# Optimization experiments

Hardware: AMD Instinct MI355X
Metric: run time of the kernel (lower is better)

Reference implementation:

```python
import jax
import jax.numpy as jnp
import numpy as np
from jax import lax

KSIZE = 3
C = 32


def _conv3x3(x, w):
    # NCHW input, OIHW weight, stride 1, padding 1 (matches nn.Conv2d(padding=1))
    return lax.conv_general_dilated(
        x, w, window_strides=(1, 1), padding=((1, 1), (1, 1)),
        dimension_numbers=("NCHW", "OIHW", "NCHW"))


def setup_inputs() -> dict:
    key = jax.random.key(0)
    k1, k2, k3 = jax.random.split(key, 3)
    N, H, W = 2, 64, 64
    x = jax.random.normal(k1, (N, C, H, W), dtype=jnp.float32)
    # conv1: C -> C, 3x3; PyTorch default init scale ~ 1/sqrt(fan_in)
    conv1_w = jax.random.normal(k2, (C, C, 3, 3), dtype=jnp.float32) * (1.0 / np.sqrt(C * 9))
    # conv2: C -> C*C*9, 3x3
    conv2_w = jax.random.normal(k3, (C * C * KSIZE * KSIZE, C, 3, 3), dtype=jnp.float32) * (1.0 / np.sqrt(C * 9))
    return {"x": x, "conv1_w": conv1_w, "conv2_w": conv2_w}


def reference(x, conv1_w, conv2_w):
    N, _, H, W = x.shape
    # kernel-generation branch: conv -> relu -> conv -> tanh
    h = jax.nn.relu(_conv3x3(x, conv1_w))
    rst = _conv3x3(h, conv2_w)  # [N, C*C*9, H, W]
    weight = jnp.tanh(rst.reshape(N, C, C, H, W, KSIZE, KSIZE))
    # non-uniform conv apply: per-pixel CxC 3x3 kernel, pad=1
    xp = jnp.pad(x, ((0, 0), (0, 0), (1, 1), (1, 1)))
    # patches[n, ci, h, w, kh, kw] = xp[n, ci, h+kh, w+kw]
    patches = jnp.stack(
        [xp[:, :, kh:kh + H, kw:kw + W] for kh in range(KSIZE) for kw in range(KSIZE)],
        axis=-1).reshape(N, C, H, W, KSIZE, KSIZE)
    out = jnp.einsum("noihwkl,nihwkl->nohw", weight, patches)
    return out
```

## Files before the change

kernel.cpp:

```cpp
#include <hip/hip_runtime.h>

typedef unsigned int uint;
typedef unsigned short ushort_t;

#define CN 32
#define HW 4096
#define KDIM 288
#define PDIM 8192
#define NB 2

typedef __attribute__((ext_vector_type(8))) short bf16x8;
typedef __attribute__((ext_vector_type(4))) float f32x4;

static __device__ __forceinline__ ushort_t f2bf(float f) {
    uint u = __float_as_uint(f);
    uint r = (u + 0x7fffu + ((u >> 16) & 1u)) >> 16;
    return (ushort_t)r;
}

static __device__ __forceinline__ void gl_lds16(const void* g, void* l) {
    __builtin_amdgcn_global_load_lds(
        (const __attribute__((address_space(1))) unsigned int*)g,
        (__attribute__((address_space(3))) unsigned int*)l, 16, 0, 0);
}

static __device__ __forceinline__ float fast_tanh(float v) {
    float e = __expf(2.0f * v);
    return 1.0f - 2.0f * __builtin_amdgcn_rcpf(e + 1.0f);
}


__global__ __launch_bounds__(256) void prep_kernel(
    const float* __restrict__ x, const float* __restrict__ w1,
    const float* __restrict__ w2, float* __restrict__ hout,
    ushort_t* __restrict__ A_bf, float4* __restrict__ out_zero)
{
    __shared__ float w1s[KDIM];
    int bb = blockIdx.x;
    if (bb < 256) {
        int c = (bb >> 2) & 31;
        int n = bb >> 7;
        for (int j = threadIdx.x; j < KDIM; j += 256) w1s[j] = w1[c * KDIM + j];
        __syncthreads();

        int idx = bb * 256 + threadIdx.x;
        int ws0 = (idx & 15) * 4;
        int hh  = (idx >> 4) & 63;

        float acc0 = 0.f, acc1 = 0.f, acc2 = 0.f, acc3 = 0.f;
        for (int ci = 0; ci < CN; ci++) {
            const float* xp = x + (((size_t)(n * CN + ci)) << 12);
            #pragma unroll
            for (int kh = 0; kh < 3; kh++) {
                int y = hh + kh - 1;
                if ((unsigned)y >= 64u) continue;
                const float* row = xp + (y << 6);
                float4 v = *(const float4*)(row + ws0);
                float left  = (ws0 > 0)  ? row[ws0 - 1] : 0.f;
                float right = (ws0 < 60) ? row[ws0 + 4] : 0.f;
                float rb[6] = {left, v.x, v.y, v.z, v.w, right};
                const float* wp = &w1s[ci * 9 + kh * 3];
                #pragma unroll
                for (int kw = 0; kw < 3; kw++) {
                    float wgt = wp[kw];
                    acc0 = fmaf(wgt, rb[0 + kw], acc0);
                    acc1 = fmaf(wgt, rb[1 + kw], acc1);
                    acc2 = fmaf(wgt, rb[2 + kw], acc2);
                    acc3 = fmaf(wgt, rb[3 + kw], acc3);
                }
            }
        }
        float4 o = make_float4(fmaxf(acc0, 0.f), fmaxf(acc1, 0.f),
                               fmaxf(acc2, 0.f), fmaxf(acc3, 0.f));
        *(float4*)(hout + (((size_t)(n * CN + c)) << 12) + (hh << 6) + ws0) = o;
    } else {
        int idx = (bb - 256) * 256 + threadIdx.x;
        if (idx < 65536)
            out_zero[idx] = make_float4(0.f, 0.f, 0.f, 0.f);
        int row = idx / 36;
        int cw  = idx - row * 36;
        int g = cw >> 2, s = cw & 3;
        const float* base = w2 + (size_t)row * KDIM + g * 32;
        float4 lo = *(const float4*)(base + s * 4);
        float4 hi = *(const float4*)(base + 16 + s * 4);
        alignas(16) ushort_t o[8] = {f2bf(lo.x), f2bf(lo.y), f2bf(lo.z), f2bf(lo.w),
                                     f2bf(hi.x), f2bf(hi.y), f2bf(hi.z), f2bf(hi.w)};
        *(uint4*)(A_bf + (size_t)idx * 8) = *(const uint4*)o;
    }
}

__global__ __launch_bounds__(256) void im2col_bf16_perm(
    const float* __restrict__ h, ushort_t* __restrict__ Bm)
{
    int idx = blockIdx.x * 256 + threadIdx.x;
    int p  = idx / 36;
    int cw = idx - p * 36;
    int g = cw >> 2, s = cw & 3;
    int n  = p >> 12;
    int sp = p & 4095;
    int hh = sp >> 6;
    int w  = sp & 63;
    const float* hn = h + (((size_t)n * CN) << 12);
    alignas(16) ushort_t o[8];
    #pragma unroll
    for (int j = 0; j < 8; j++) {
        int ko = (j < 4) ? (s * 4 + j) : (12 + s * 4 + j);
        int k  = g * 32 + ko;
        int ci = (k * 57) >> 9;
        int kk = k - ci * 9;
        int kh = (kk * 11) >> 5;
        int kw = kk - kh * 3;
        int y  = hh + kh - 1;
        int xw = w + kw - 1;
        float v = 0.f;
        if ((unsigned)y < 64u && (unsigned)xw < 64u)
            v = hn[((size_t)ci << 12) + (y << 6) + xw];
        o[j] = f2bf(v);
    }
    *(uint4*)(Bm + (size_t)idx * 8) = *(const uint4*)o;
}

__global__ __launch_bounds__(512, 4) void fused_gemm_apply(
    const ushort_t* __restrict__ A, const ushort_t* __restrict__ B,
    const float* __restrict__ x, float* __restrict__ out)
{
    __shared__ ushort_t AL[2][128 * 32];
    __shared__ ushort_t BL[2][256 * 32];
    __shared__ float vred[4][256];

    int tid = threadIdx.x;
    int bid = blockIdx.x;
    int sb  = (bid & 7) * 288 + (bid >> 3);
    int tw  = sb % 144;
    int cg  = (sb / 144) & 7;
    int n   = sb / 1152;

    int lane = tid & 63, wv = tid >> 6;
    int wm = wv >> 2, wt = wv & 3;
    int i16 = lane & 15, kg = lane >> 4;

    int T0 = tw * 256;
    int c8 = T0 >> 12;
    int q0 = T0 & 4095;

    int cA = tid;
    int rA = cA >> 2;
    int k8A = (((cA & 3) ^ ((cA >> 3) & 3)) << 3);
    const ushort_t* srcA = A +
        (size_t)((cg * 4 + (rA >> 5)) * KDIM + (rA & 31) * 9 + c8) * KDIM + k8A;
    int cB0 = tid, cB1 = 512 + tid;
    int rB0 = cB0 >> 2, rB1 = cB1 >> 2;
    int k8B0 = (((cB0 & 3) ^ ((cB0 >> 3) & 3)) << 3);
    int k8B1 = (((cB1 & 3) ^ ((cB1 >> 3) & 3)) << 3);
    const ushort_t* srcB0 = B + (size_t)((n << 12) + q0 + rB0) * KDIM + k8B0;
    const ushort_t* srcB1 = B + (size_t)((n << 12) + q0 + rB1) * KDIM + k8B1;
    int dstA = wv * 512;
    int dstB0 = wv * 512, dstB1 = 4096 + wv * 512;

    f32x4 acc[4][4] = {};

    gl_lds16(srcA,  &AL[0][dstA]);
    gl_lds16(srcB0, &BL[0][dstB0]);
    gl_lds16(srcB1, &BL[0][dstB1]);

    #pragma unroll
    for (int ks = 0; ks < 9; ks++) {
        int cur = ks & 1;
        if (ks < 8) {
            int k0 = (ks + 1) * 32;
            gl_lds16(srcA + k0,  &AL[cur ^ 1][dstA]);
            gl_lds16(srcB0 + k0, &BL[cur ^ 1][dstB0]);
            gl_lds16(srcB1 + k0, &BL[cur ^ 1][dstB1]);
            __builtin_amdgcn_sched_barrier(0);
            asm volatile("s_waitcnt vmcnt(3)" ::: "memory");
        } else {
            __builtin_amdgcn_sched_barrier(0);
            asm volatile("s_waitcnt vmcnt(0)" ::: "memory");
        }
        __builtin_amdgcn_sched_barrier(0);
        __builtin_amdgcn_s_barrier();
        __builtin_amdgcn_sched_barrier(0);

        bf16x8 af[4], bfr[4];
        #pragma unroll
        for (int mf = 0; mf < 4; mf++) {
            int row = wm * 64 + mf * 16 + i16;
            af[mf] = *(const bf16x8*)
                &AL[cur][row * 32 + ((kg ^ ((row >> 1) & 3)) << 3)];
        }
        #pragma unroll
        for (int nf = 0; nf < 4; nf++) {
            int row = wt * 64 + nf * 16 + i16;
            bfr[nf] = *(const bf16x8*)
                &BL[cur][row * 32 + ((kg ^ ((row >> 1) & 3)) << 3)];
        }
        #pragma unroll
        for (int mf = 0; mf < 4; mf++)
            #pragma unroll
            for (int nf = 0; nf < 4; nf++)
                acc[mf][nf] = __builtin_amdgcn_mfma_f32_16x16x32_bf16(
                    af[mf], bfr[nf], acc[mf][nf], 0, 0, 0);

        __builtin_amdgcn_sched_barrier(0);
        asm volatile("s_waitcnt lgkmcnt(0)" ::: "memory");
        __builtin_amdgcn_sched_barrier(0);
        __builtin_amdgcn_s_barrier();
        __builtin_amdgcn_sched_barrier(0);
    }

    const float* xn = x + (((size_t)n * CN) << 12);
    #pragma unroll
    for (int nf = 0; nf < 4; nf++) {
        int t  = T0 + wt * 64 + nf * 16 + i16;
        uint sp = ((uint)t * 58255u) >> 19;
        int kk = t - (int)sp * 9;
        int kh = (kk * 11) >> 5;
        int kw = kk - kh * 3;
        int y  = (int)(sp >> 6) + kh - 1;
        int xw = (int)(sp & 63) + kw - 1;
        bool ok = ((unsigned)y < 64u) && ((unsigned)xw < 64u);
        int poff = (y << 6) + xw;
        float xa[4], xb[4];
        #pragma unroll
        for (int r = 0; r < 4; r++) {
            int cia = kg * 4 + r;
            xa[r] = ok ? xn[((size_t)cia << 12) + poff] : 0.f;
            xb[r] = ok ? xn[((size_t)(cia + 16) << 12) + poff] : 0.f;
        }
        float s0 = 0.f, s1 = 0.f;
        #pragma unroll
        for (int r = 0; r < 4; r++) {
            s0 = fmaf(fast_tanh(acc[0][nf][r]), xa[r], s0);
            s0 = fmaf(fast_tanh(acc[1][nf][r]), xb[r], s0);
            s1 = fmaf(fast_tanh(acc[2][nf][r]), xa[r], s1);
            s1 = fmaf(fast_tanh(acc[3][nf][r]), xb[r], s1);
        }
        s0 += __shfl_xor(s0, 16); s0 += __shfl_xor(s0, 32);
        s1 += __shfl_xor(s1, 16); s1 += __shfl_xor(s1, 32);
        if (kg == 0) {
            vred[2 * wm + 0][wt * 64 + nf * 16 + i16] = s0;
            vred[2 * wm + 1][wt * 64 + nf * 16 + i16] = s1;
        }
    }
    __syncthreads();

    if (tid < 128) {
        int g  = tid >> 5, bi = tid & 31;
        uint spA = ((uint)T0 * 58255u) >> 19;
        int sp = (int)spA + bi;
        int lo = sp * 9;     if (lo < T0) lo = T0;
        int hi = sp * 9 + 9; if (hi > T0 + 256) hi = T0 + 256;
        if (lo < hi) {
            float s = 0.f;
            for (int t = lo; t < hi; t++) s += vred[g][t - T0];
            atomicAdd(&out[(((size_t)n * CN + cg * 4 + g) << 12) + sp], s);
        }
    }
}

extern "C" void kernel_launch(void* const* d_in, const int* in_sizes, int n_in,
                              void* d_out, int out_size, void* d_ws, size_t ws_size,
                              hipStream_t stream) {
    const float* x  = (const float*)d_in[0];
    const float* w1 = (const float*)d_in[1];
    const float* w2 = (const float*)d_in[2];
    float* out = (float*)d_out;
    char* ws = (char*)d_ws;

    float*    hbuf  = (float*)ws;
    ushort_t* Bm_bf = (ushort_t*)(ws + 1048576u);
    ushort_t* A_bf  = (ushort_t*)(ws + 5767168u);

    hipLaunchKernelGGL(prep_kernel, dim3(1552), dim3(256), 0, stream,
                       x, w1, w2, hbuf, A_bf, (float4*)out);
    hipLaunchKernelGGL(im2col_bf16_perm, dim3(1152), dim3(256), 0,
                       stream, hbuf, Bm_bf);
    hipLaunchKernelGGL(fused_gemm_apply, dim3(2304), dim3(512), 0, stream,
                       A_bf, Bm_bf, x, out);
}
```

Measured before the change: 114.5 us.

## Triple-buffer GEMM LDS loads and split conv1 channel reduction across threads

The fused GEMM moves from double to triple buffering, issuing loads two k-steps ahead with adjusted vmcnt waits so global-to-LDS latency is hidden better. The conv1 part of the prep kernel now launches twice as many blocks. Each block splits the input channels into two halves, and the partial sums are reduced through shared memory before the ReLU. The extra LDS per block (48KB for the buffers) may lower occupancy in the GEMM, which has launch bounds of 4 blocks per multiprocessor.

```diff
diff --git a/kernel.cpp b/kernel.cpp
--- a/kernel.cpp
+++ b/kernel.cpp
@@ -36,19 +36,24 @@
     ushort_t* __restrict__ A_bf, float4* __restrict__ out_zero)
 {
     __shared__ float w1s[KDIM];
+    __shared__ float ps[2][128][4];
     int bb = blockIdx.x;
-    if (bb < 256) {
-        int c = (bb >> 2) & 31;
-        int n = bb >> 7;
-        for (int j = threadIdx.x; j < KDIM; j += 256) w1s[j] = w1[c * KDIM + j];
+    int tid = threadIdx.x;
+    if (bb < 512) {
+        int n  = bb >> 8;
+        int c  = (bb >> 3) & 31;
+        int rg = bb & 7;
+        for (int j = tid; j < KDIM; j += 256) w1s[j] = w1[c * KDIM + j];
         __syncthreads();
 
-        int idx = bb * 256 + threadIdx.x;
-        int ws0 = (idx & 15) * 4;
-        int hh  = (idx >> 4) & 63;
+        int half = tid >> 7;
+        int i2   = tid & 127;
+        int hh   = rg * 8 + (i2 >> 4);
+        int ws0  = (i2 & 15) * 4;
 
         float acc0 = 0.f, acc1 = 0.f, acc2 = 0.f, acc3 = 0.f;
-        for (int ci = 0; ci < CN; ci++) {
+        int ci0 = half * 16;
+        for (int ci = ci0; ci < ci0 + 16; ci++) {
             const float* xp = x + (((size_t)(n * CN + ci)) << 12);
             #pragma unroll
             for (int kh = 0; kh < 3; kh++) {
@@ -70,11 +75,19 @@
                 }
             }
         }
-        float4 o = make_float4(fmaxf(acc0, 0.f), fmaxf(acc1, 0.f),
-                               fmaxf(acc2, 0.f), fmaxf(acc3, 0.f));
-        *(float4*)(hout + (((size_t)(n * CN + c)) << 12) + (hh << 6) + ws0) = o;
+        ps[half][i2][0] = acc0; ps[half][i2][1] = acc1;
+        ps[half][i2][2] = acc2; ps[half][i2][3] = acc3;
+        __syncthreads();
+        if (half == 0) {
+            float4 o = make_float4(
+                fmaxf(ps[0][i2][0] + ps[1][i2][0], 0.f),
+                fmaxf(ps[0][i2][1] + ps[1][i2][1], 0.f),
+                fmaxf(ps[0][i2][2] + ps[1][i2][2], 0.f),
+                fmaxf(ps[0][i2][3] + ps[1][i2][3], 0.f));
+            *(float4*)(hout + (((size_t)(n * CN + c)) << 12) + (hh << 6) + ws0) = o;
+        }
     } else {
-        int idx = (bb - 256) * 256 + threadIdx.x;
+        int idx = (bb - 512) * 256 + tid;
         if (idx < 65536)
             out_zero[idx] = make_float4(0.f, 0.f, 0.f, 0.f);
         int row = idx / 36;
@@ -124,8 +137,8 @@
     const ushort_t* __restrict__ A, const ushort_t* __restrict__ B,
     const float* __restrict__ x, float* __restrict__ out)
 {
-    __shared__ ushort_t AL[2][128 * 32];
-    __shared__ ushort_t BL[2][256 * 32];
+    __shared__ ushort_t AL[3][128 * 32];
+    __shared__ ushort_t BL[3][256 * 32];
     __shared__ float vred[4][256];
 
     int tid = threadIdx.x;
@@ -154,23 +167,28 @@
     int k8B1 = (((cB1 & 3) ^ ((cB1 >> 3) & 3)) << 3);
     const ushort_t* srcB0 = B + (size_t)((n << 12) + q0 + rB0) * KDIM + k8B0;
     const ushort_t* srcB1 = B + (size_t)((n << 12) + q0 + rB1) * KDIM + k8B1;
-    int dstA = wv * 512;
-    int dstB0 = wv * 512, dstB1 = 4096 + wv * 512;
+    int dstA = wv * 512, dstB0 = wv * 512, dstB1 = 4096 + wv * 512;
+
+#define STAGE(BUF, KS)                                                  \
+    do { int _k0 = (KS) * 32;                                           \
+        gl_lds16(srcA + _k0,  &AL[BUF][dstA]);                          \
+        gl_lds16(srcB0 + _k0, &BL[BUF][dstB0]);                         \
+        gl_lds16(srcB1 + _k0, &BL[BUF][dstB1]);                         \
+    } while (0)
 
     f32x4 acc[4][4] = {};
 
-    gl_lds16(srcA,  &AL[0][dstA]);
-    gl_lds16(srcB0, &BL[0][dstB0]);
-    gl_lds16(srcB1, &BL[0][dstB1]);
+    STAGE(0, 0);
+    STAGE(1, 1);
 
     #pragma unroll
     for (int ks = 0; ks < 9; ks++) {
-        int cur = ks & 1;
-        if (ks < 8) {
-            int k0 = (ks + 1) * 32;
-            gl_lds16(srcA + k0,  &AL[cur ^ 1][dstA]);
-            gl_lds16(srcB0 + k0, &BL[cur ^ 1][dstB0]);
-            gl_lds16(srcB1 + k0, &BL[cur ^ 1][dstB1]);
+        int cur = ks % 3;
+        if (ks < 7) {
+            STAGE((ks + 2) % 3, ks + 2);
+            __builtin_amdgcn_sched_barrier(0);
+            asm volatile("s_waitcnt vmcnt(6)" ::: "memory");
+        } else if (ks == 7) {
             __builtin_amdgcn_sched_barrier(0);
             asm volatile("s_waitcnt vmcnt(3)" ::: "memory");
         } else {
@@ -207,6 +225,7 @@
         __builtin_amdgcn_s_barrier();
         __builtin_amdgcn_sched_barrier(0);
     }
+#undef STAGE
 
     const float* xn = x + (((size_t)n * CN) << 12);
     #pragma unroll
@@ -271,7 +290,7 @@
     ushort_t* Bm_bf = (ushort_t*)(ws + 1048576u);
     ushort_t* A_bf  = (ushort_t*)(ws + 5767168u);
 
-    hipLaunchKernelGGL(prep_kernel, dim3(1552), dim3(256), 0, stream,
+    hipLaunchKernelGGL(prep_kernel, dim3(1808), dim3(256), 0, stream,
                        x, w1, w2, hbuf, A_bf, (float4*)out);
     hipLaunchKernelGGL(im2col_bf16_perm, dim3(1152), dim3(256), 0,
                        stream, hbuf, Bm_bf);
```

Measured after the change: 98.17 us. -14.3%, faster.
